# Kernel tuning notes

Hardware: AMD Instinct MI355X
Metric: run time of the kernel (lower is better)

## Reference

```python
import jax, jax.numpy as jnp
import numpy as np

N_NODES = 1_000_000
D_IN = 64
D_HID = 64
NUM_RATINGS = 10


def setup_inputs() -> dict:
    key = jax.random.key(0)
    k1, k2, k3, k4 = jax.random.split(key, 4)
    embed = jax.random.normal(k1, (N_NODES, D_IN), dtype=jnp.float32)
    # rating-indexed weight matrices W_r : (hidden_size, input_size)
    weights = jax.random.normal(k2, (NUM_RATINGS, D_HID, D_IN), dtype=jnp.float32)
    # precomputed 1/c_ij per edge (sqrt of neighbor-count product inverse)
    inv_c = jax.random.uniform(k3, (N_NODES,), dtype=jnp.float32)
    edge_node = jnp.arange(N_NODES, dtype=jnp.int64)
    edge_rating = jax.random.randint(k4, (N_NODES,), 0, NUM_RATINGS, dtype=jnp.int64)
    return {"embed": embed, "weights": weights, "inv_c": inv_c,
            "edge_node": edge_node, "edge_rating": edge_rating}


def reference(embed, weights, inv_c, edge_node, edge_rating):
    # gather per-edge source embeddings: [E, D_in]
    x = embed[edge_node]
    num_ratings, d_hid, _ = weights.shape
    # rating-specific matvec without materializing per-edge [Dh, Din] weights:
    # loop over the small fixed rating set, select per edge.
    h = jnp.zeros((x.shape[0], d_hid), dtype=x.dtype)
    for r in range(num_ratings):
        yr = x @ weights[r].T  # [E, Dh]
        h = jnp.where((edge_rating == r)[:, None], yr, h)
    h = h * inv_c[:, None]
    out = jnp.zeros((embed.shape[0], d_hid), dtype=x.dtype).at[edge_node].set(h)
    return out
```

## Files before the change

### kernel.cpp

```cpp
#include <hip/hip_runtime.h>
#include <hip/hip_bf16.h>

#define NUM_RATINGS 10

typedef short bf16x8 __attribute__((ext_vector_type(8)));
typedef float f32x4 __attribute__((ext_vector_type(4)));

static __device__ __forceinline__ bf16x8 rne8(float4 a, float4 b) {
    float f[8] = {a.x, a.y, a.z, a.w, b.x, b.y, b.z, b.w};
    union { unsigned short us[8]; bf16x8 v; } U;
    #pragma unroll
    for (int i = 0; i < 8; ++i) {
        unsigned u = __float_as_uint(f[i]);
        U.us[i] = (unsigned short)((u + 0x7fffu + ((u >> 16) & 1u)) >> 16);
    }
    return U.v;
}

__global__ void k_wfrag(const float* __restrict__ w, bf16x8* __restrict__ wf) {
    int r = blockIdx.x;
    int lane = threadIdx.x & 63;
    int eh = lane & 15, kg = lane >> 4;
    #pragma unroll
    for (int j = 0; j < 8; ++j) {
        int tt = j >> 1, ks = j & 1;
        const float4* p = reinterpret_cast<const float4*>(
            w + ((size_t)r << 12) + (size_t)(16 * tt + eh) * 64 + 32 * ks + 8 * kg);
        wf[(r * 8 + j) * 64 + lane] = rne8(p[0], p[1]);
    }
}

__global__ __launch_bounds__(256) void k_main(
    const float* __restrict__ embed, const bf16x8* __restrict__ wf,
    const float* __restrict__ invc, const int* __restrict__ enode,
    const int* __restrict__ erating, float* __restrict__ out, int E) {

    int lane = threadIdx.x & 63;
    int wv = threadIdx.x >> 6;
    int eh = lane & 15, kg = lane >> 4;
    int e0 = (blockIdx.x * 4 + wv) * 64;
    if (e0 >= E) return;

    int nd[4]; int rt[4]; float sc[4];
    #pragma unroll
    for (int it = 0; it < 4; ++it) {
        int et = e0 + 16 * it + eh;
        if (et > E - 1) et = E - 1;
        nd[it] = enode[et];
        rt[it] = erating[et];
        sc[it] = invc[et];
    }

    bf16x8 a0[4], a1[4];
    #pragma unroll
    for (int it = 0; it < 4; ++it) {
        const float4* xp = reinterpret_cast<const float4*>(embed + ((size_t)nd[it] << 6));
        float4 x0 = xp[2 * kg],     x1 = xp[2 * kg + 1];
        float4 x2 = xp[8 + 2 * kg], x3 = xp[9 + 2 * kg];
        a0[it] = rne8(x0, x1);
        a1[it] = rne8(x2, x3);
    }

    f32x4 acc[4][4];
    #pragma unroll
    for (int it = 0; it < 4; ++it)
        #pragma unroll
        for (int tt = 0; tt < 4; ++tt) acc[it][tt] = (f32x4){0.f, 0.f, 0.f, 0.f};

    #pragma unroll 1
    for (int r = 0; r < NUM_RATINGS; ++r) {
        bf16x8 B[8];
        #pragma unroll
        for (int j = 0; j < 8; ++j) B[j] = wf[(r * 8 + j) * 64 + lane];
        #pragma unroll
        for (int it = 0; it < 4; ++it) {
            bool m = (rt[it] == r);
            bf16x8 z = (bf16x8)(short)0;
            bf16x8 am0 = m ? a0[it] : z;
            bf16x8 am1 = m ? a1[it] : z;
            #pragma unroll
            for (int tt = 0; tt < 4; ++tt) {
                acc[it][tt] = __builtin_amdgcn_mfma_f32_16x16x32_bf16(am0, B[2 * tt],     acc[it][tt], 0, 0, 0);
                acc[it][tt] = __builtin_amdgcn_mfma_f32_16x16x32_bf16(am1, B[2 * tt + 1], acc[it][tt], 0, 0, 0);
            }
        }
    }

    int kg4 = kg << 2;
    #pragma unroll
    for (int it = 0; it < 4; ++it) {
        #pragma unroll
        for (int rg = 0; rg < 4; ++rg) {
            int er = e0 + 16 * it + kg4 + rg;
            int nd2 = __shfl(nd[it], kg4 + rg, 64);
            float s2 = __shfl(sc[it], kg4 + rg, 64);
            if (er < E) {
                float* po = out + ((size_t)nd2 << 6) + eh;
                __builtin_nontemporal_store(acc[it][0][rg] * s2, po);
                __builtin_nontemporal_store(acc[it][1][rg] * s2, po + 16);
                __builtin_nontemporal_store(acc[it][2][rg] * s2, po + 32);
                __builtin_nontemporal_store(acc[it][3][rg] * s2, po + 48);
            }
        }
    }
}

extern "C" void kernel_launch(void* const* d_in, const int* in_sizes, int n_in,
                              void* d_out, int out_size, void* d_ws, size_t ws_size,
                              hipStream_t stream) {
    const float* embed   = (const float*)d_in[0];
    const float* weights = (const float*)d_in[1];
    const float* invc    = (const float*)d_in[2];
    const int*   enode   = (const int*)d_in[3];
    const int*   erating = (const int*)d_in[4];
    float* out = (float*)d_out;

    int E = in_sizes[3];

    bf16x8* wf = (bf16x8*)d_ws;

    hipLaunchKernelGGL(k_wfrag, dim3(NUM_RATINGS), dim3(64), 0, stream, weights, wf);

    int waves = (E + 63) / 64;
    int blocks = (waves + 3) / 4;
    hipLaunchKernelGGL(k_main, dim3(blocks), dim3(256), 0, stream,
                       embed, wf, invc, enode, erating, out, E);
}
```

Before: 129.3 us.

## Persistent waves with software-pipelined gathers, LDS weights, and rating-presence skipping

The main kernel becomes a persistent grid of 2048 waves that each walk 32-edge chunks, prefetching edge metadata two chunks ahead and embeddings one chunk ahead so gathers overlap with MFMA work. Weight fragments are staged once per block into shared memory rather than read from global memory per rating. A wave-level presence mask skips MFMAs for ratings absent from its edges, and the inv_c scale is folded into the bf16 conversion of the inputs instead of being applied to outputs. This trades more registers and a fixed grid size for better latency hiding and fewer wasted MFMAs. Scaling before rounding slightly changes numerics.

```diff
diff --git a/kernel.cpp b/kernel.cpp
--- a/kernel.cpp
+++ b/kernel.cpp
@@ -2,6 +2,7 @@
 #include <hip/hip_bf16.h>
 
 #define NUM_RATINGS 10
+#define GW 2048
 
 typedef short bf16x8 __attribute__((ext_vector_type(8)));
 typedef float f32x4 __attribute__((ext_vector_type(4)));
@@ -12,6 +13,17 @@
     #pragma unroll
     for (int i = 0; i < 8; ++i) {
         unsigned u = __float_as_uint(f[i]);
+        U.us[i] = (unsigned short)((u + 0x7fffu + ((u >> 16) & 1u)) >> 16);
+    }
+    return U.v;
+}
+
+static __device__ __forceinline__ bf16x8 rne8s(float4 a, float4 b, float s) {
+    float f[8] = {a.x, a.y, a.z, a.w, b.x, b.y, b.z, b.w};
+    union { unsigned short us[8]; bf16x8 v; } U;
+    #pragma unroll
+    for (int i = 0; i < 8; ++i) {
+        unsigned u = __float_as_uint(f[i] * s);
         U.us[i] = (unsigned short)((u + 0x7fffu + ((u >> 16) & 1u)) >> 16);
     }
     return U.v;
@@ -30,78 +42,127 @@
     }
 }
 
-__global__ __launch_bounds__(256) void k_main(
+#define MLOAD(S, CC) { \
+    int cc_ = (CC); if (cc_ > NCm1) cc_ = NCm1; \
+    int b_ = cc_ * 32 + eh; \
+    int ea_ = b_ > Em1 ? Em1 : b_; \
+    int eb_ = (b_ + 16) > Em1 ? Em1 : (b_ + 16); \
+    nd##S##0 = enode[ea_]; rt##S##0 = erating[ea_]; sc##S##0 = invc[ea_]; \
+    nd##S##1 = enode[eb_]; rt##S##1 = erating[eb_]; sc##S##1 = invc[eb_]; }
+
+#define XLOADM(XS, MS) { \
+    const float4* pa_ = reinterpret_cast<const float4*>(embed + ((size_t)nd##MS##0 << 6)); \
+    const float4* pb_ = reinterpret_cast<const float4*>(embed + ((size_t)nd##MS##1 << 6)); \
+    x##XS##00 = pa_[2 * kg]; x##XS##01 = pa_[2 * kg + 1]; \
+    x##XS##02 = pa_[8 + 2 * kg]; x##XS##03 = pa_[9 + 2 * kg]; \
+    x##XS##10 = pb_[2 * kg]; x##XS##11 = pb_[2 * kg + 1]; \
+    x##XS##12 = pb_[8 + 2 * kg]; x##XS##13 = pb_[9 + 2 * kg]; }
+
+#define ITER(MP, MQ, XC, XN) { \
+    XLOADM(XN, MQ) \
+    int snd0 = nd##MP##0, snd1 = nd##MP##1; \
+    int srt0 = rt##MP##0, srt1 = rt##MP##1; \
+    float ssc0 = sc##MP##0, ssc1 = sc##MP##1; \
+    bf16x8 a00 = rne8s(x##XC##00, x##XC##01, ssc0); \
+    bf16x8 a01 = rne8s(x##XC##02, x##XC##03, ssc0); \
+    bf16x8 a10 = rne8s(x##XC##10, x##XC##11, ssc1); \
+    bf16x8 a11 = rne8s(x##XC##12, x##XC##13, ssc1); \
+    MLOAD(MP, c + 2 * GW) \
+    unsigned pres0 = 0, pres1 = 0; \
+    _Pragma("unroll") \
+    for (int rq = 0; rq < NUM_RATINGS; ++rq) { \
+        if (__any(srt0 == rq)) pres0 |= 1u << rq; \
+        if (__any(srt1 == rq)) pres1 |= 1u << rq; \
+    } \
+    f32x4 ac0[4], ac1[4]; \
+    _Pragma("unroll") \
+    for (int t_ = 0; t_ < 4; ++t_) { \
+        ac0[t_] = (f32x4){0.f, 0.f, 0.f, 0.f}; \
+        ac1[t_] = (f32x4){0.f, 0.f, 0.f, 0.f}; \
+    } \
+    _Pragma("unroll 1") \
+    for (int r_ = 0; r_ < NUM_RATINGS; ++r_) { \
+        if (!(((pres0 | pres1) >> r_) & 1u)) continue; \
+        bf16x8 Bv[8]; \
+        _Pragma("unroll") \
+        for (int j_ = 0; j_ < 8; ++j_) Bv[j_] = swf[(r_ * 8 + j_) * 64 + lane]; \
+        bf16x8 z_ = (bf16x8)(short)0; \
+        if ((pres0 >> r_) & 1u) { \
+            bf16x8 m0_ = (srt0 == r_) ? a00 : z_; \
+            bf16x8 m1_ = (srt0 == r_) ? a01 : z_; \
+            _Pragma("unroll") \
+            for (int t_ = 0; t_ < 4; ++t_) { \
+                ac0[t_] = __builtin_amdgcn_mfma_f32_16x16x32_bf16(m0_, Bv[2 * t_],     ac0[t_], 0, 0, 0); \
+                ac0[t_] = __builtin_amdgcn_mfma_f32_16x16x32_bf16(m1_, Bv[2 * t_ + 1], ac0[t_], 0, 0, 0); \
+            } \
+        } \
+        if ((pres1 >> r_) & 1u) { \
+            bf16x8 m0_ = (srt1 == r_) ? a10 : z_; \
+            bf16x8 m1_ = (srt1 == r_) ? a11 : z_; \
+            _Pragma("unroll") \
+            for (int t_ = 0; t_ < 4; ++t_) { \
+                ac1[t_] = __builtin_amdgcn_mfma_f32_16x16x32_bf16(m0_, Bv[2 * t_],     ac1[t_], 0, 0, 0); \
+                ac1[t_] = __builtin_amdgcn_mfma_f32_16x16x32_bf16(m1_, Bv[2 * t_ + 1], ac1[t_], 0, 0, 0); \
+            } \
+        } \
+    } \
+    int kg4 = kg << 2; \
+    _Pragma("unroll") \
+    for (int rg = 0; rg < 4; ++rg) { \
+        int er0 = c * 32 + kg4 + rg; \
+        int nda = __shfl(snd0, kg4 + rg, 64); \
+        if (er0 < E) { \
+            float* po = out + ((size_t)nda << 6) + eh; \
+            __builtin_nontemporal_store(ac0[0][rg], po); \
+            __builtin_nontemporal_store(ac0[1][rg], po + 16); \
+            __builtin_nontemporal_store(ac0[2][rg], po + 32); \
+            __builtin_nontemporal_store(ac0[3][rg], po + 48); \
+        } \
+        int er1 = c * 32 + 16 + kg4 + rg; \
+        int ndb = __shfl(snd1, kg4 + rg, 64); \
+        if (er1 < E) { \
+            float* po = out + ((size_t)ndb << 6) + eh; \
+            __builtin_nontemporal_store(ac1[0][rg], po); \
+            __builtin_nontemporal_store(ac1[1][rg], po + 16); \
+            __builtin_nontemporal_store(ac1[2][rg], po + 32); \
+            __builtin_nontemporal_store(ac1[3][rg], po + 48); \
+        } \
+    } \
+}
+
+__global__ __launch_bounds__(256, 2) void k_main(
     const float* __restrict__ embed, const bf16x8* __restrict__ wf,
     const float* __restrict__ invc, const int* __restrict__ enode,
     const int* __restrict__ erating, float* __restrict__ out, int E) {
 
+    __shared__ bf16x8 swf[NUM_RATINGS * 8 * 64];
+    for (int i = threadIdx.x; i < NUM_RATINGS * 8 * 64; i += 256)
+        swf[i] = wf[i];
+    __syncthreads();
+
     int lane = threadIdx.x & 63;
     int wv = threadIdx.x >> 6;
     int eh = lane & 15, kg = lane >> 4;
-    int e0 = (blockIdx.x * 4 + wv) * 64;
-    if (e0 >= E) return;
 
-    int nd[4]; int rt[4]; float sc[4];
-    #pragma unroll
-    for (int it = 0; it < 4; ++it) {
-        int et = e0 + 16 * it + eh;
-        if (et > E - 1) et = E - 1;
-        nd[it] = enode[et];
-        rt[it] = erating[et];
-        sc[it] = invc[et];
-    }
+    int NC = (E + 31) >> 5;
+    int NCm1 = NC - 1, Em1 = E - 1;
+    int c = blockIdx.x * 4 + wv;
+    if (c >= NC) return;
 
-    bf16x8 a0[4], a1[4];
-    #pragma unroll
-    for (int it = 0; it < 4; ++it) {
-        const float4* xp = reinterpret_cast<const float4*>(embed + ((size_t)nd[it] << 6));
-        float4 x0 = xp[2 * kg],     x1 = xp[2 * kg + 1];
-        float4 x2 = xp[8 + 2 * kg], x3 = xp[9 + 2 * kg];
-        a0[it] = rne8(x0, x1);
-        a1[it] = rne8(x2, x3);
-    }
+    int ndP0, ndP1, rtP0, rtP1; float scP0, scP1;
+    int ndQ0, ndQ1, rtQ0, rtQ1; float scQ0, scQ1;
+    float4 xX00, xX01, xX02, xX03, xX10, xX11, xX12, xX13;
+    float4 xY00, xY01, xY02, xY03, xY10, xY11, xY12, xY13;
 
-    f32x4 acc[4][4];
-    #pragma unroll
-    for (int it = 0; it < 4; ++it)
-        #pragma unroll
-        for (int tt = 0; tt < 4; ++tt) acc[it][tt] = (f32x4){0.f, 0.f, 0.f, 0.f};
+    MLOAD(P, c)
+    MLOAD(Q, c + GW)
+    XLOADM(X, P)
 
-    #pragma unroll 1
-    for (int r = 0; r < NUM_RATINGS; ++r) {
-        bf16x8 B[8];
-        #pragma unroll
-        for (int j = 0; j < 8; ++j) B[j] = wf[(r * 8 + j) * 64 + lane];
-        #pragma unroll
-        for (int it = 0; it < 4; ++it) {
-            bool m = (rt[it] == r);
-            bf16x8 z = (bf16x8)(short)0;
-            bf16x8 am0 = m ? a0[it] : z;
-            bf16x8 am1 = m ? a1[it] : z;
-            #pragma unroll
-            for (int tt = 0; tt < 4; ++tt) {
-                acc[it][tt] = __builtin_amdgcn_mfma_f32_16x16x32_bf16(am0, B[2 * tt],     acc[it][tt], 0, 0, 0);
-                acc[it][tt] = __builtin_amdgcn_mfma_f32_16x16x32_bf16(am1, B[2 * tt + 1], acc[it][tt], 0, 0, 0);
-            }
-        }
-    }
-
-    int kg4 = kg << 2;
-    #pragma unroll
-    for (int it = 0; it < 4; ++it) {
-        #pragma unroll
-        for (int rg = 0; rg < 4; ++rg) {
-            int er = e0 + 16 * it + kg4 + rg;
-            int nd2 = __shfl(nd[it], kg4 + rg, 64);
-            float s2 = __shfl(sc[it], kg4 + rg, 64);
-            if (er < E) {
-                float* po = out + ((size_t)nd2 << 6) + eh;
-                __builtin_nontemporal_store(acc[it][0][rg] * s2, po);
-                __builtin_nontemporal_store(acc[it][1][rg] * s2, po + 16);
-                __builtin_nontemporal_store(acc[it][2][rg] * s2, po + 32);
-                __builtin_nontemporal_store(acc[it][3][rg] * s2, po + 48);
-            }
-        }
+    while (1) {
+        ITER(P, Q, X, Y)
+        c += GW; if (c >= NC) break;
+        ITER(Q, P, Y, X)
+        c += GW; if (c >= NC) break;
     }
 }
 
@@ -120,9 +181,6 @@
     bf16x8* wf = (bf16x8*)d_ws;
 
     hipLaunchKernelGGL(k_wfrag, dim3(NUM_RATINGS), dim3(64), 0, stream, weights, wf);
-
-    int waves = (E + 63) / 64;
-    int blocks = (waves + 3) / 4;
-    hipLaunchKernelGGL(k_main, dim3(blocks), dim3(256), 0, stream,
+    hipLaunchKernelGGL(k_main, dim3(GW / 4), dim3(256), 0, stream,
                        embed, wf, invc, enode, erating, out, E);
 }
```

After: 116.2 us. 10.1% less time.
